# Kernel tuning notes

Hardware: AMD Instinct MI355X
Metric: run time of the kernel (lower is better)

Reference implementation:

```python
import jax, jax.numpy as jnp
import numpy as np

B, S, D = 4, 2048, 1024


def setup_inputs() -> dict:
    key = jax.random.key(0)
    kx, kq, kk, kv, km = jax.random.split(key, 5)
    bound = 1.0 / np.sqrt(D)  # torch Linear default init range
    X = jax.random.normal(kx, (B, S, D), dtype=jnp.float32)
    Wq = jax.random.uniform(kq, (D, D), jnp.float32, -bound, bound)
    Wk = jax.random.uniform(kk, (D, D), jnp.float32, -bound, bound)
    Wv = jax.random.uniform(kv, (D, D), jnp.float32, -bound, bound)
    masks = jax.random.randint(km, (B, S), 0, 2, dtype=jnp.int32)
    return {"X": X, "masks": masks, "Wq": Wq, "Wk": Wk, "Wv": Wv}


def reference(X, masks, Wq, Wk, Wv):
    n = X.shape[1]
    # mask construction: True where masked (padding OR future position)
    lookahead = jnp.triu(jnp.ones((n, n), dtype=bool), k=1)          # [S,S]
    pad = ~(masks.astype(bool))[:, None, :]                           # [B,1,S] -> key-side padding
    m = (pad | lookahead[None]).astype(X.dtype)                       # [B,S,S]

    # Linear layers (torch: y = x @ W.T)
    Q = jnp.einsum('bsd,ed->bse', X, Wq)
    K = jnp.einsum('bsd,ed->bse', X, Wk)
    V = jnp.einsum('bsd,ed->bse', X, Wv)

    # cosine-normalized attention scores, multiplied (not added) by the mask
    Qn = Q / jnp.linalg.norm(Q, axis=-1, keepdims=True)
    Kn = K / jnp.linalg.norm(K, axis=-1, keepdims=True)
    scores = jnp.einsum('bqd,bkd->bqk', Qn, Kn) * m                   # [B,S,S]
    return jnp.einsum('bqk,bkd->bqd', scores, V)
```

## Files before the change

### kernel.cpp

```cpp
#include <hip/hip_runtime.h>
#include <hip/hip_bf16.h>

#define B_ 4
#define S_ 2048
#define D_ 1024
#define MTOT (B_ * S_)

typedef __attribute__((ext_vector_type(8))) short bf16x8;
typedef __attribute__((ext_vector_type(4))) float f32x4;

__device__ __forceinline__ unsigned short f2bf(float f) {
  union { float f; unsigned int u; } v; v.f = f;
  unsigned int r = v.u + 0x7FFFu + ((v.u >> 16) & 1u);
  return (unsigned short)(r >> 16);
}
__device__ __forceinline__ float bf2f(unsigned short u) {
  union { unsigned int u; float f; } v; v.u = ((unsigned int)u) << 16;
  return v.f;
}

__global__ void cvt_f32_bf16(const float* __restrict__ in, unsigned short* __restrict__ outp, int n4) {
  int i = blockIdx.x * blockDim.x + threadIdx.x;
  if (i >= n4) return;
  float4 v = ((const float4*)in)[i];
  ushort4 o;
  o.x = f2bf(v.x); o.y = f2bf(v.y); o.z = f2bf(v.z); o.w = f2bf(v.w);
  ((ushort4*)outp)[i] = o;
}

__global__ __launch_bounds__(256) void rownorm_bf16(const unsigned short* __restrict__ QKb,
                                                    unsigned short* __restrict__ Qn,
                                                    unsigned short* __restrict__ Kn) {
  int row = blockIdx.x;
  int half = blockIdx.y;
  int tid = threadIdx.x;
  ushort4 u = *(const ushort4*)(QKb + (long)row * 2048 + half * 1024 + tid * 4);
  float x0 = bf2f(u.x), x1 = bf2f(u.y), x2 = bf2f(u.z), x3 = bf2f(u.w);
  float ss = x0 * x0 + x1 * x1 + x2 * x2 + x3 * x3;
#pragma unroll
  for (int o = 1; o < 64; o <<= 1) ss += __shfl_xor(ss, o);
  __shared__ float wsum[4];
  if ((tid & 63) == 0) wsum[tid >> 6] = ss;
  __syncthreads();
  float rn = rsqrtf(wsum[0] + wsum[1] + wsum[2] + wsum[3]);
  ushort4 o;
  o.x = f2bf(x0 * rn); o.y = f2bf(x1 * rn); o.z = f2bf(x2 * rn); o.w = f2bf(x3 * rn);
  unsigned short* op = half ? Kn : Qn;
  *(ushort4*)(op + (long)row * D_ + tid * 4) = o;
}

#define BM 128
#define BN 128
#define BK 32

#define GLDS16(g, l)                                                                   \
  __builtin_amdgcn_global_load_lds((const __attribute__((address_space(1))) void*)(g), \
                                   (__attribute__((address_space(3))) void*)(l), 16, 0, 0)

template <int EPI>
__global__ __launch_bounds__(256, 2) void gemm_bt(const unsigned short* __restrict__ A,
                                                  const unsigned short* __restrict__ B,
                                                  void* __restrict__ Cv, int N, int K,
                                                  long strideA, long strideB, long strideC,
                                                  const int* __restrict__ masks) {
  __shared__ __align__(16) short lA[2][BM * BK];
  __shared__ __align__(16) short lB[2][BN * BK];
  int z = blockIdx.z;
  const unsigned short* Ab = A + (long)z * strideA;
  const unsigned short* Bb = B + (long)z * strideB;
  int tid = threadIdx.x;
  int lane = tid & 63, w = tid >> 6;
  int wr = w >> 1, wc = w & 1;
  int brow = blockIdx.x * BM, bcol = blockIdx.y * BN;

  f32x4 acc[4][4];
#pragma unroll
  for (int m = 0; m < 4; m++)
#pragma unroll
    for (int n = 0; n < 4; n++) acc[m][n] = (f32x4){0.f, 0.f, 0.f, 0.f};

  const unsigned short* ga = Ab + (long)(brow + (tid >> 2)) * K + ((tid & 3) << 3);
  const unsigned short* gb = Bb + (long)(bcol + (tid >> 2)) * K + ((tid & 3) << 3);
  int fr = lane & 15, fq = lane >> 4;

#define STAGE(buf)                                          \
  do {                                                      \
    char* la = (char*)(&lA[buf][0]) + ((tid >> 6) << 10);   \
    char* lb = (char*)(&lB[buf][0]) + ((tid >> 6) << 10);   \
    GLDS16(ga, la);                                         \
    GLDS16(ga + (long)64 * K, la + 4096);                   \
    GLDS16(gb, lb);                                         \
    GLDS16(gb + (long)64 * K, lb + 4096);                   \
    ga += BK;                                               \
    gb += BK;                                               \
  } while (0)

  STAGE(0);
  __syncthreads();

  int nt = K / BK;
  for (int t = 0; t < nt; ++t) {
    int cur = t & 1;
    if (t + 1 < nt) STAGE(cur ^ 1);
    const short* pa = &lA[cur][(wr * 64 + fr) * BK + fq * 8];
    const short* pb = &lB[cur][(wc * 64 + fr) * BK + fq * 8];
    bf16x8 af[4], bv[4];
#pragma unroll
    for (int m = 0; m < 4; m++) af[m] = *(const bf16x8*)(pa + m * 16 * BK);
#pragma unroll
    for (int n = 0; n < 4; n++) bv[n] = *(const bf16x8*)(pb + n * 16 * BK);
#pragma unroll
    for (int m = 0; m < 4; m++)
#pragma unroll
      for (int n = 0; n < 4; n++)
        acc[m][n] = __builtin_amdgcn_mfma_f32_16x16x32_bf16(af[m], bv[n], acc[m][n], 0, 0, 0);
    __syncthreads();
  }
#undef STAGE

  long cbase = (long)z * strideC;
#pragma unroll
  for (int m = 0; m < 4; m++) {
#pragma unroll
    for (int n = 0; n < 4; n++) {
#pragma unroll
      for (int r = 0; r < 4; r++) {
        int grow = brow + wr * 64 + m * 16 + fq * 4 + r;
        int gcol = bcol + wc * 64 + n * 16 + fr;
        float v = acc[m][n][r];
        if constexpr (EPI == 0) {
          ((float*)Cv)[cbase + (long)grow * N + gcol] = v;
        } else if constexpr (EPI == 1) {
          ((unsigned short*)Cv)[cbase + (long)grow * N + gcol] = f2bf(v);
        } else if constexpr (EPI == 2) {
          bool keep = (gcol > grow) || (masks[z * S_ + gcol] == 0);
          ((unsigned short*)Cv)[cbase + (long)grow * N + gcol] = keep ? f2bf(v) : (unsigned short)0;
        } else {
          int b = gcol >> 11, s = gcol & (S_ - 1);
          ((unsigned short*)Cv)[(long)b * D_ * S_ + (long)grow * S_ + s] = f2bf(v);
        }
      }
    }
  }
}

extern "C" void kernel_launch(void* const* d_in, const int* in_sizes, int n_in, void* d_out,
                              int out_size, void* d_ws, size_t ws_size, hipStream_t stream) {
  (void)in_sizes; (void)n_in; (void)out_size; (void)ws_size;
  const float* X = (const float*)d_in[0];
  const int* masks = (const int*)d_in[1];
  const float* Wq = (const float*)d_in[2];
  const float* Wk = (const float*)d_in[3];
  const float* Wv = (const float*)d_in[4];
  float* out = (float*)d_out;

  char* ws = (char*)d_ws;
  unsigned short* Xb = (unsigned short*)ws;   ws += (long)MTOT * D_ * 2;
  unsigned short* Wqkb = (unsigned short*)ws; ws += (long)2 * D_ * D_ * 2;
  unsigned short* Wvb = (unsigned short*)ws;  ws += (long)D_ * D_ * 2;
  unsigned short* QKb = (unsigned short*)ws;  ws += (long)MTOT * 2 * D_ * 2;
  unsigned short* Qn = (unsigned short*)ws;   ws += (long)MTOT * D_ * 2;
  unsigned short* Kn = (unsigned short*)ws;   ws += (long)MTOT * D_ * 2;
  unsigned short* Vt = (unsigned short*)ws;   ws += (long)MTOT * D_ * 2;
  unsigned short* Sm = (unsigned short*)ws;   ws += (long)B_ * S_ * S_ * 2;

  int n4x = MTOT * D_ / 4;
  cvt_f32_bf16<<<(n4x + 255) / 256, 256, 0, stream>>>(X, Xb, n4x);
  int n4w = D_ * D_ / 4;
  cvt_f32_bf16<<<(n4w + 255) / 256, 256, 0, stream>>>(Wq, Wqkb, n4w);
  cvt_f32_bf16<<<(n4w + 255) / 256, 256, 0, stream>>>(Wk, Wqkb + (long)D_ * D_, n4w);
  cvt_f32_bf16<<<(n4w + 255) / 256, 256, 0, stream>>>(Wv, Wvb, n4w);

  dim3 blk(256);
  gemm_bt<1><<<dim3(MTOT / BM, 2 * D_ / BN, 1), blk, 0, stream>>>(Xb, Wqkb, QKb, 2 * D_, D_,
                                                                  0, 0, 0, nullptr);
  rownorm_bf16<<<dim3(MTOT, 2), 256, 0, stream>>>(QKb, Qn, Kn);
  gemm_bt<3><<<dim3(D_ / BM, MTOT / BN, 1), blk, 0, stream>>>(Wvb, Xb, Vt, MTOT, D_,
                                                              0, 0, 0, nullptr);
  gemm_bt<2><<<dim3(S_ / BM, S_ / BN, B_), blk, 0, stream>>>(Qn, Kn, Sm, S_, D_,
                                                             (long)S_ * D_, (long)S_ * D_,
                                                             (long)S_ * S_, masks);
  gemm_bt<0><<<dim3(S_ / BM, D_ / BN, B_), blk, 0, stream>>>(Sm, Vt, out, D_, S_,
                                                             (long)S_ * S_, (long)D_ * S_,
                                                             (long)S_ * D_, nullptr);
}
```

Measured before the change: 201.2 us.

## Replace GEMM with 256x256 tile, 8-wave, swizzled-LDS ping-pong MFMA kernel

Replaces the 128x128x32, 4-wave GEMM with a 256x256x64 tile kernel of 8 waves that uses 128KB of dynamic LDS. Rows are XOR-swizzled in LDS to avoid bank conflicts, and the loop interleaves quarter-tile LDS reads with MFMA bursts under explicit barriers and s_setprio. The K dimension is a template parameter so the loop can be fully scheduled. The aim is more data reuse per byte loaded and better overlap of loads with matrix math. In exchange, the larger tiles mean fewer blocks per grid, for example only 128 blocks for the V projection, and occupancy is limited by LDS.

```diff
diff --git a/kernel.cpp b/kernel.cpp
--- a/kernel.cpp
+++ b/kernel.cpp
@@ -49,85 +49,155 @@
   *(ushort4*)(op + (long)row * D_ + tid * 4) = o;
 }
 
-#define BM 128
-#define BN 128
-#define BK 32
 
 #define GLDS16(g, l)                                                                   \
   __builtin_amdgcn_global_load_lds((const __attribute__((address_space(1))) void*)(g), \
                                    (__attribute__((address_space(3))) void*)(l), 16, 0, 0)
 
-template <int EPI>
-__global__ __launch_bounds__(256, 2) void gemm_bt(const unsigned short* __restrict__ A,
-                                                  const unsigned short* __restrict__ B,
-                                                  void* __restrict__ Cv, int N, int K,
-                                                  long strideA, long strideB, long strideC,
-                                                  const int* __restrict__ masks) {
-  __shared__ __align__(16) short lA[2][BM * BK];
-  __shared__ __align__(16) short lB[2][BN * BK];
-  int z = blockIdx.z;
+template <int EPI, int KK>
+__global__ __launch_bounds__(512, 2) void gemm8(const unsigned short* __restrict__ A,
+                                                const unsigned short* __restrict__ B,
+                                                void* __restrict__ Cv, int N,
+                                                long strideA, long strideB, long strideC,
+                                                const int* __restrict__ masks) {
+  constexpr int NT = KK / 64;
+  extern __shared__ __align__(16) char smem[];
+  char* smA = smem;
+  char* smB = smem + 65536;
+
+  const int z = blockIdx.z;
   const unsigned short* Ab = A + (long)z * strideA;
   const unsigned short* Bb = B + (long)z * strideB;
-  int tid = threadIdx.x;
-  int lane = tid & 63, w = tid >> 6;
-  int wr = w >> 1, wc = w & 1;
-  int brow = blockIdx.x * BM, bcol = blockIdx.y * BN;
-
-  f32x4 acc[4][4];
-#pragma unroll
-  for (int m = 0; m < 4; m++)
+  const int t = threadIdx.x;
+  const int lane = t & 63, w = t >> 6;
+  const int wm = w >> 2, wn = w & 3;
+  const int fr = lane & 15, fq = lane >> 4;
+  const int brow = blockIdx.x * 256, bcol = blockIdx.y * 256;
+
+  const int srow = t >> 3;
+  const int sswz = ((t & 7) * 16) ^ ((srow & 7) << 4);
+  const char* gA = (const char*)(Ab + (long)(brow + srow) * KK) + sswz;
+  const char* gB = (const char*)(Bb + (long)(bcol + srow) * KK) + sswz;
+  const long jstr = (long)64 * KK * 2;
+
+#define STAGE8(kt2, bf)                                   \
+  do {                                                    \
+    const char* ga_ = gA + (long)(kt2) * 128;             \
+    const char* gb_ = gB + (long)(kt2) * 128;             \
+    char* la_ = smA + (bf) * 32768 + t * 16;              \
+    char* lb_ = smB + (bf) * 32768 + t * 16;              \
+    GLDS16(ga_, la_);                                     \
+    GLDS16(ga_ + jstr, la_ + 8192);                       \
+    GLDS16(ga_ + 2 * jstr, la_ + 16384);                  \
+    GLDS16(ga_ + 3 * jstr, la_ + 24576);                  \
+    GLDS16(gb_, lb_);                                     \
+    GLDS16(gb_ + jstr, lb_ + 8192);                       \
+    GLDS16(gb_ + 2 * jstr, lb_ + 16384);                  \
+    GLDS16(gb_ + 3 * jstr, lb_ + 24576);                  \
+  } while (0)
+
+  const int c0 = (fq * 16) ^ ((fr & 7) << 4);
+  const int c1 = c0 ^ 64;
+  const int arow = (wm * 128 + fr) * 128;
+  const int brw = (wn * 64 + fr) * 128;
+
+  f32x4 acc[8][4];
+#pragma unroll
+  for (int m = 0; m < 8; m++)
 #pragma unroll
     for (int n = 0; n < 4; n++) acc[m][n] = (f32x4){0.f, 0.f, 0.f, 0.f};
-
-  const unsigned short* ga = Ab + (long)(brow + (tid >> 2)) * K + ((tid & 3) << 3);
-  const unsigned short* gb = Bb + (long)(bcol + (tid >> 2)) * K + ((tid & 3) << 3);
-  int fr = lane & 15, fq = lane >> 4;
-
-#define STAGE(buf)                                          \
-  do {                                                      \
-    char* la = (char*)(&lA[buf][0]) + ((tid >> 6) << 10);   \
-    char* lb = (char*)(&lB[buf][0]) + ((tid >> 6) << 10);   \
-    GLDS16(ga, la);                                         \
-    GLDS16(ga + (long)64 * K, la + 4096);                   \
-    GLDS16(gb, lb);                                         \
-    GLDS16(gb + (long)64 * K, lb + 4096);                   \
-    ga += BK;                                               \
-    gb += BK;                                               \
-  } while (0)
-
-  STAGE(0);
-  __syncthreads();
-
-  int nt = K / BK;
-  for (int t = 0; t < nt; ++t) {
-    int cur = t & 1;
-    if (t + 1 < nt) STAGE(cur ^ 1);
-    const short* pa = &lA[cur][(wr * 64 + fr) * BK + fq * 8];
-    const short* pb = &lB[cur][(wc * 64 + fr) * BK + fq * 8];
-    bf16x8 af[4], bv[4];
-#pragma unroll
-    for (int m = 0; m < 4; m++) af[m] = *(const bf16x8*)(pa + m * 16 * BK);
-#pragma unroll
-    for (int n = 0; n < 4; n++) bv[n] = *(const bf16x8*)(pb + n * 16 * BK);
-#pragma unroll
-    for (int m = 0; m < 4; m++)
-#pragma unroll
-      for (int n = 0; n < 4; n++)
-        acc[m][n] = __builtin_amdgcn_mfma_f32_16x16x32_bf16(af[m], bv[n], acc[m][n], 0, 0, 0);
-    __syncthreads();
+  bf16x8 af[4][2], bv[2][2][2];
+
+#define LDA(qm)                                                               \
+  do {                                                                        \
+    _Pragma("unroll") for (int mf = 0; mf < 4; ++mf) {                        \
+      af[mf][0] = *(const bf16x8*)(pa + c0 + (((qm)*64 + mf * 16) << 7));     \
+      af[mf][1] = *(const bf16x8*)(pa + c1 + (((qm)*64 + mf * 16) << 7));     \
+    }                                                                         \
+  } while (0)
+
+#define LDB(qn)                                                               \
+  do {                                                                        \
+    _Pragma("unroll") for (int nf = 0; nf < 2; ++nf) {                        \
+      bv[(qn)][nf][0] = *(const bf16x8*)(pb + c0 + (((qn)*32 + nf * 16) << 7)); \
+      bv[(qn)][nf][1] = *(const bf16x8*)(pb + c1 + (((qn)*32 + nf * 16) << 7)); \
+    }                                                                         \
+  } while (0)
+
+#define MFMAQ(qm, qn)                                                         \
+  do {                                                                        \
+    _Pragma("unroll") for (int ks = 0; ks < 2; ++ks)                          \
+    _Pragma("unroll") for (int nf = 0; nf < 2; ++nf)                          \
+    _Pragma("unroll") for (int mf = 0; mf < 4; ++mf)                          \
+      acc[(qm)*4 + mf][(qn)*2 + nf] = __builtin_amdgcn_mfma_f32_16x16x32_bf16(\
+          af[mf][ks], bv[(qn)][nf][ks], acc[(qm)*4 + mf][(qn)*2 + nf], 0, 0, 0); \
+  } while (0)
+
+#define BARW()                                                \
+  do {                                                        \
+    __builtin_amdgcn_s_barrier();                             \
+    asm volatile("s_waitcnt lgkmcnt(0)" ::: "memory");        \
+    __builtin_amdgcn_sched_barrier(0);                        \
+  } while (0)
+
+  STAGE8(0, 0);
+  STAGE8(1, 1);
+  asm volatile("s_waitcnt vmcnt(8)" ::: "memory");
+  __builtin_amdgcn_s_barrier();
+
+#pragma unroll 2
+  for (int kt = 0; kt < NT; ++kt) {
+    const int cur = kt & 1;
+    const char* pa = smA + cur * 32768 + arow;
+    const char* pb = smB + cur * 32768 + brw;
+    LDA(0);
+    LDB(0);
+    BARW();
+    __builtin_amdgcn_s_setprio(1);
+    MFMAQ(0, 0);
+    __builtin_amdgcn_s_setprio(0);
+    __builtin_amdgcn_s_barrier();
+    LDB(1);
+    BARW();
+    __builtin_amdgcn_s_setprio(1);
+    MFMAQ(0, 1);
+    __builtin_amdgcn_s_setprio(0);
+    __builtin_amdgcn_s_barrier();
+    LDA(1);
+    BARW();
+    __builtin_amdgcn_s_setprio(1);
+    MFMAQ(1, 1);
+    __builtin_amdgcn_s_setprio(0);
+    __builtin_amdgcn_s_barrier();
+    if (kt + 2 < NT) STAGE8(kt + 2, cur);
+    BARW();
+    __builtin_amdgcn_s_setprio(1);
+    MFMAQ(1, 0);
+    __builtin_amdgcn_s_setprio(0);
+    if (kt + 1 < NT) {
+      if (kt + 2 < NT)
+        asm volatile("s_waitcnt vmcnt(8)" ::: "memory");
+      else
+        asm volatile("s_waitcnt vmcnt(0)" ::: "memory");
+      __builtin_amdgcn_s_barrier();
+    }
   }
-#undef STAGE
+#undef STAGE8
+#undef LDA
+#undef LDB
+#undef MFMAQ
+#undef BARW
 
   long cbase = (long)z * strideC;
 #pragma unroll
-  for (int m = 0; m < 4; m++) {
-#pragma unroll
-    for (int n = 0; n < 4; n++) {
-#pragma unroll
-      for (int r = 0; r < 4; r++) {
-        int grow = brow + wr * 64 + m * 16 + fq * 4 + r;
-        int gcol = bcol + wc * 64 + n * 16 + fr;
-        float v = acc[m][n][r];
+  for (int Mi = 0; Mi < 8; ++Mi) {
+#pragma unroll
+    for (int Ni = 0; Ni < 4; ++Ni) {
+#pragma unroll
+      for (int r = 0; r < 4; ++r) {
+        int grow = brow + wm * 128 + Mi * 16 + fq * 4 + r;
+        int gcol = bcol + wn * 64 + Ni * 16 + fr;
+        float v = acc[Mi][Ni][r];
         if constexpr (EPI == 0) {
           ((float*)Cv)[cbase + (long)grow * N + gcol] = v;
         } else if constexpr (EPI == 1) {
@@ -164,6 +234,12 @@
   unsigned short* Vt = (unsigned short*)ws;   ws += (long)MTOT * D_ * 2;
   unsigned short* Sm = (unsigned short*)ws;   ws += (long)B_ * S_ * S_ * 2;
 
+  constexpr unsigned SMEM = 131072;
+  (void)hipFuncSetAttribute((const void*)gemm8<1, 1024>, hipFuncAttributeMaxDynamicSharedMemorySize, SMEM);
+  (void)hipFuncSetAttribute((const void*)gemm8<3, 1024>, hipFuncAttributeMaxDynamicSharedMemorySize, SMEM);
+  (void)hipFuncSetAttribute((const void*)gemm8<2, 1024>, hipFuncAttributeMaxDynamicSharedMemorySize, SMEM);
+  (void)hipFuncSetAttribute((const void*)gemm8<0, 2048>, hipFuncAttributeMaxDynamicSharedMemorySize, SMEM);
+
   int n4x = MTOT * D_ / 4;
   cvt_f32_bf16<<<(n4x + 255) / 256, 256, 0, stream>>>(X, Xb, n4x);
   int n4w = D_ * D_ / 4;
@@ -171,16 +247,13 @@
   cvt_f32_bf16<<<(n4w + 255) / 256, 256, 0, stream>>>(Wk, Wqkb + (long)D_ * D_, n4w);
   cvt_f32_bf16<<<(n4w + 255) / 256, 256, 0, stream>>>(Wv, Wvb, n4w);
 
-  dim3 blk(256);
-  gemm_bt<1><<<dim3(MTOT / BM, 2 * D_ / BN, 1), blk, 0, stream>>>(Xb, Wqkb, QKb, 2 * D_, D_,
-                                                                  0, 0, 0, nullptr);
+  gemm8<1, 1024><<<dim3(MTOT / 256, 2 * D_ / 256, 1), 512, SMEM, stream>>>(
+      Xb, Wqkb, QKb, 2 * D_, 0, 0, 0, nullptr);
   rownorm_bf16<<<dim3(MTOT, 2), 256, 0, stream>>>(QKb, Qn, Kn);
-  gemm_bt<3><<<dim3(D_ / BM, MTOT / BN, 1), blk, 0, stream>>>(Wvb, Xb, Vt, MTOT, D_,
-                                                              0, 0, 0, nullptr);
-  gemm_bt<2><<<dim3(S_ / BM, S_ / BN, B_), blk, 0, stream>>>(Qn, Kn, Sm, S_, D_,
-                                                             (long)S_ * D_, (long)S_ * D_,
-                                                             (long)S_ * S_, masks);
-  gemm_bt<0><<<dim3(S_ / BM, D_ / BN, B_), blk, 0, stream>>>(Sm, Vt, out, D_, S_,
-                                                             (long)S_ * S_, (long)D_ * S_,
-                                                             (long)S_ * D_, nullptr);
-}
+  gemm8<3, 1024><<<dim3(D_ / 256, MTOT / 256, 1), 512, SMEM, stream>>>(
+      Wvb, Xb, Vt, MTOT, 0, 0, 0, nullptr);
+  gemm8<2, 1024><<<dim3(S_ / 256, S_ / 256, B_), 512, SMEM, stream>>>(
+      Qn, Kn, Sm, S_, (long)S_ * D_, (long)S_ * D_, (long)S_ * S_, masks);
+  gemm8<0, 2048><<<dim3(S_ / 256, D_ / 256, B_), 512, SMEM, stream>>>(
+      Sm, Vt, out, D_, (long)S_ * S_, (long)D_ * S_, (long)S_ * D_, nullptr);
+}
```

After: 217.9 us. 1.08x slower.
